# Kernel tuning notes

Hardware: AMD Instinct MI355X
Metric: run time of the kernel (lower is better)

The kernel has to match this reference:

```python
import jax, jax.numpy as jnp
import numpy as np

N = 50000   # nodes
E = 600000  # edges
D = 128     # hidden dim (all layers)
LN_EPS = 1e-5


def setup_inputs() -> dict:
    key = jax.random.key(0)
    ks = jax.random.split(key, 12)
    s = 1.0 / np.sqrt(D)
    inp = {
        "x": jax.random.normal(ks[0], (N, D), jnp.float32),
        "edge_index": jax.random.randint(ks[1], (2, E), 0, N, dtype=jnp.int64),
    }
    # per-layer params: SAGEConv lin_l (W+b, applied to aggregated neighbors),
    # lin_r (W only, applied to root/self), LayerNorm gamma/beta
    for i in range(2):
        inp[f"W_l{i}"] = jax.random.normal(ks[2 + 5 * i], (D, D), jnp.float32) * s
        inp[f"b_l{i}"] = jnp.zeros((D,), jnp.float32)
        inp[f"W_r{i}"] = jax.random.normal(ks[3 + 5 * i], (D, D), jnp.float32) * s
        inp[f"gamma{i}"] = jnp.ones((D,), jnp.float32)
        inp[f"beta{i}"] = jnp.zeros((D,), jnp.float32)
    return inp


def _sage_layer(x, src, dst, W_l, b_l, W_r, gamma, beta):
    n = x.shape[0]
    # mean-aggregate source features at destination nodes (PyG SAGEConv 'mean')
    msg = x[src]                                                # [E, D] gather
    summed = jax.ops.segment_sum(msg, dst, num_segments=n)      # [N, D] scatter-add
    cnt = jax.ops.segment_sum(jnp.ones_like(dst, dtype=x.dtype), dst, num_segments=n)
    agg = summed / jnp.maximum(cnt, 1.0)[:, None]               # zero for isolated nodes
    out = agg @ W_l.T + b_l + x @ W_r.T                         # lin_l(agg) + lin_r(x)
    # LayerNorm + ReLU (dropout=None, negative_slope=None -> ReLU)
    mu = jnp.mean(out, axis=-1, keepdims=True)
    var = jnp.var(out, axis=-1, keepdims=True)
    out = (out - mu) * jax.lax.rsqrt(var + LN_EPS) * gamma + beta
    return jax.nn.relu(out)


def reference(x, edge_index, W_l0, b_l0, W_r0, gamma0, beta0,
              W_l1, b_l1, W_r1, gamma1, beta1):
    src, dst = edge_index[0], edge_index[1]
    x = _sage_layer(x, src, dst, W_l0, b_l0, W_r0, gamma0, beta0)
    x = _sage_layer(x, src, dst, W_l1, b_l1, W_r1, gamma1, beta1)
    return x
```

## Files before the change

### kernel.cpp

```cpp
#include <hip/hip_runtime.h>

#define D 128
#define BR 128

typedef _Float16 f16;
typedef f16 f16x8 __attribute__((ext_vector_type(8)));
typedef float f32x4 __attribute__((ext_vector_type(4)));

__global__ void zero_kernel(int4* __restrict__ p, int count4) {
    const int i = blockIdx.x * 256 + threadIdx.x;
    if (i < count4) p[i] = make_int4(0, 0, 0, 0);
}

__global__ void convert_kernel(const float* __restrict__ src, f16* __restrict__ dst,
                               int count8) {
    const int i = blockIdx.x * 256 + threadIdx.x;
    if (i >= count8) return;
    const float4 v0 = *(const float4*)(src + (size_t)i * 8);
    const float4 v1 = *(const float4*)(src + (size_t)i * 8 + 4);
    f16x8 h;
    h[0] = (f16)v0.x; h[1] = (f16)v0.y; h[2] = (f16)v0.z; h[3] = (f16)v0.w;
    h[4] = (f16)v1.x; h[5] = (f16)v1.y; h[6] = (f16)v1.z; h[7] = (f16)v1.w;
    *(f16x8*)(dst + (size_t)i * 8) = h;
}

__global__ void count_kernel(const int* __restrict__ dst, int* __restrict__ cnt, int E) {
    int e = blockIdx.x * 256 + threadIdx.x;
    if (e < E) atomicAdd(&cnt[dst[e]], 1);
}

__global__ __launch_bounds__(256)
void scan1_kernel(const int* __restrict__ cnt, int* __restrict__ part, int n) {
    const int t = threadIdx.x;
    const int i0 = blockIdx.x * 1024 + t * 4;
    int s = 0;
#pragma unroll
    for (int j = 0; j < 4; ++j) { int i = i0 + j; if (i < n) s += cnt[i]; }
#pragma unroll
    for (int m = 1; m < 64; m <<= 1) s += __shfl_xor(s, m, 64);
    __shared__ int ws[4];
    if ((t & 63) == 0) ws[t >> 6] = s;
    __syncthreads();
    if (t == 0) part[blockIdx.x] = ws[0] + ws[1] + ws[2] + ws[3];
}

__global__ __launch_bounds__(256)
void scan3_kernel(const int* __restrict__ cnt, const int* __restrict__ part,
                  int* __restrict__ off, int* __restrict__ cursor, int n, int nb) {
    const int t = threadIdx.x;
    const int lane = t & 63, wid = t >> 6;
    __shared__ int s_base;
    if (t < 64) {
        int s = 0;
        for (int base = 0; base < nb; base += 64) {
            const int idx = base + lane;
            if (idx < nb && idx < (int)blockIdx.x) s += part[idx];
        }
#pragma unroll
        for (int m = 1; m < 64; m <<= 1) s += __shfl_xor(s, m, 64);
        if (lane == 0) s_base = s;
    }
    const int i0 = blockIdx.x * 1024 + t * 4;
    int v[4]; int s = 0;
#pragma unroll
    for (int j = 0; j < 4; ++j) { v[j] = (i0 + j < n) ? cnt[i0 + j] : 0; s += v[j]; }
    int incl = s;
#pragma unroll
    for (int m = 1; m < 64; m <<= 1) {
        int u = __shfl_up(incl, m, 64);
        if (lane >= m) incl += u;
    }
    __shared__ int ws[4];
    if (lane == 63) ws[wid] = incl;
    __syncthreads();
    int woff = 0;
#pragma unroll
    for (int k = 0; k < 4; ++k) woff += (k < wid) ? ws[k] : 0;
    int run = s_base + woff + incl - s;
#pragma unroll
    for (int j = 0; j < 4; ++j) {
        if (i0 + j < n) { off[i0 + j] = run; cursor[i0 + j] = run; run += v[j]; }
    }
}

__global__ void fill_kernel(const int* __restrict__ src, const int* __restrict__ dst,
                            int* cursor, int* __restrict__ adj, int E) {
    int e = blockIdx.x * 256 + threadIdx.x;
    if (e < E) {
        int pos = atomicAdd(&cursor[dst[e]], 1);
        adj[pos] = src[e];
    }
}

__global__ __launch_bounds__(256, 8)
void aggregate_kernel(const f16* xin, const int* __restrict__ adj,
                      const int* __restrict__ off, const int* __restrict__ cnt,
                      f16* __restrict__ agg, int n) {
    const int node = blockIdx.x * 16 + (threadIdx.x >> 4);
    if (node >= n) return;
    const int lane = threadIdx.x & 15;
    const int deg = cnt[node];
    const int o = off[node];
    const f16* xp = xin + (lane << 3);
    float a0 = 0.f, a1 = 0.f, a2 = 0.f, a3 = 0.f;
    float a4 = 0.f, a5 = 0.f, a6 = 0.f, a7 = 0.f;
    int k = 0;
    for (; k + 8 <= deg; k += 8) {
        int sidx[8];
#pragma unroll
        for (int j = 0; j < 8; ++j) sidx[j] = adj[o + k + j];
#pragma unroll
        for (int j = 0; j < 8; ++j) {
            const f16x8 v = *(const f16x8*)(xp + (size_t)sidx[j] * D);
            a0 += (float)v[0]; a1 += (float)v[1]; a2 += (float)v[2]; a3 += (float)v[3];
            a4 += (float)v[4]; a5 += (float)v[5]; a6 += (float)v[6]; a7 += (float)v[7];
        }
    }
    for (; k + 4 <= deg; k += 4) {
        int sidx[4];
#pragma unroll
        for (int j = 0; j < 4; ++j) sidx[j] = adj[o + k + j];
#pragma unroll
        for (int j = 0; j < 4; ++j) {
            const f16x8 v = *(const f16x8*)(xp + (size_t)sidx[j] * D);
            a0 += (float)v[0]; a1 += (float)v[1]; a2 += (float)v[2]; a3 += (float)v[3];
            a4 += (float)v[4]; a5 += (float)v[5]; a6 += (float)v[6]; a7 += (float)v[7];
        }
    }
    for (; k < deg; ++k) {
        const f16x8 v = *(const f16x8*)(xp + (size_t)adj[o + k] * D);
        a0 += (float)v[0]; a1 += (float)v[1]; a2 += (float)v[2]; a3 += (float)v[3];
        a4 += (float)v[4]; a5 += (float)v[5]; a6 += (float)v[6]; a7 += (float)v[7];
    }
    const float s = 1.0f / (float)max(deg, 1);
    f16x8 r;
    r[0] = (f16)(a0 * s); r[1] = (f16)(a1 * s);
    r[2] = (f16)(a2 * s); r[3] = (f16)(a3 * s);
    r[4] = (f16)(a4 * s); r[5] = (f16)(a5 * s);
    r[6] = (f16)(a6 * s); r[7] = (f16)(a7 * s);
    *(f16x8*)(agg + (size_t)node * D + (lane << 3)) = r;
}

__device__ __forceinline__ void stage_tile_h(const f16* src, f16* dst,
                                             int row0, int n, int tid) {
#pragma unroll
    for (int i = 0; i < 4; ++i) {
        const int flat = i * 4096 + tid * 8;
        const int row = flat >> 7;
        const int k = flat & 127;
        f16x8 h = {};
        if (row0 + row < n) h = *(const f16x8*)(src + (size_t)(row0 + row) * D + k);
        *(f16x8*)(dst + row * D + (k ^ ((row & 7) * 8))) = h;
    }
}

__device__ __forceinline__ void stage_w(const float* __restrict__ src, f16* dst, int tid) {
#pragma unroll
    for (int i = 0; i < 4; ++i) {
        const int flat = i * 4096 + tid * 8;
        const int row = flat >> 7;
        const int k = flat & 127;
        const float4 v0 = *(const float4*)(src + flat);
        const float4 v1 = *(const float4*)(src + flat + 4);
        f16x8 h;
        h[0] = (f16)v0.x; h[1] = (f16)v0.y; h[2] = (f16)v0.z; h[3] = (f16)v0.w;
        h[4] = (f16)v1.x; h[5] = (f16)v1.y; h[6] = (f16)v1.z; h[7] = (f16)v1.w;
        *(f16x8*)(dst + row * D + (k ^ ((row & 7) * 8))) = h;
    }
}

template <bool LAST>
__global__ __launch_bounds__(512, 2)
void fused_kernel(const f16* __restrict__ aggh, const f16* xinh,
                  const float* __restrict__ Wl, const float* __restrict__ bl,
                  const float* __restrict__ Wr,
                  const float* __restrict__ gamma, const float* __restrict__ beta,
                  f16* yh, float* __restrict__ yf, int n) {
    extern __shared__ char lds_raw[];
    f16* As = (f16*)lds_raw;
    f16* Ws = (f16*)(lds_raw + 32768);
    const int tid = threadIdx.x;
    const int w = tid >> 6, l = tid & 63;
    const int c = l & 15, g = l >> 4;
    const int row0 = blockIdx.x * BR;

    f32x4 acc[8];
#pragma unroll
    for (int jt = 0; jt < 8; ++jt) acc[jt] = (f32x4){0.f, 0.f, 0.f, 0.f};

    for (int pass = 0; pass < 2; ++pass) {
        if (pass) __syncthreads();
        stage_tile_h(pass ? xinh : aggh, As, row0, n, tid);
        stage_w(pass ? Wr : Wl, Ws, tid);
        __syncthreads();
#pragma unroll
        for (int ks = 0; ks < 4; ++ks) {
            const int ke = ks * 32 + g * 8;
            const int ar = w * 16 + c;
            const f16x8 av = *(const f16x8*)(As + ar * D + (ke ^ ((ar & 7) * 8)));
            f16x8 bv[8];
#pragma unroll
            for (int jt = 0; jt < 8; ++jt) {
                const int br = jt * 16 + c;
                bv[jt] = *(const f16x8*)(Ws + br * D + (ke ^ ((br & 7) * 8)));
            }
#pragma unroll
            for (int jt = 0; jt < 8; ++jt)
                acc[jt] = __builtin_amdgcn_mfma_f32_16x16x32_f16(
                    av, bv[jt], acc[jt], 0, 0, 0);
        }
    }

    float bj[8], gj[8], btj[8];
#pragma unroll
    for (int jt = 0; jt < 8; ++jt) {
        const int j = jt * 16 + c;
        bj[jt] = bl[j]; gj[jt] = gamma[j]; btj[jt] = beta[j];
    }
#pragma unroll
    for (int reg = 0; reg < 4; ++reg) {
        float v[8]; float s1 = 0.f, s2 = 0.f;
#pragma unroll
        for (int jt = 0; jt < 8; ++jt) {
            v[jt] = acc[jt][reg] + bj[jt];
            s1 += v[jt];
            s2 = fmaf(v[jt], v[jt], s2);
        }
#pragma unroll
        for (int m = 1; m < 16; m <<= 1) {
            s1 += __shfl_xor(s1, m, 64);
            s2 += __shfl_xor(s2, m, 64);
        }
        const float mu = s1 * (1.f / 128.f);
        const float var = s2 * (1.f / 128.f) - mu * mu;
        const float rstd = rsqrtf(var + 1e-5f);
        const int row = row0 + w * 16 + g * 4 + reg;
        if (row < n) {
#pragma unroll
            for (int jt = 0; jt < 8; ++jt) {
                const float o = fmaxf((v[jt] - mu) * rstd * gj[jt] + btj[jt], 0.f);
                if (LAST) yf[(size_t)row * D + jt * 16 + c] = o;
                else      yh[(size_t)row * D + jt * 16 + c] = (f16)o;
            }
        }
    }
}

extern "C" void kernel_launch(void* const* d_in, const int* in_sizes, int n_in,
                              void* d_out, int out_size, void* d_ws, size_t ws_size,
                              hipStream_t stream) {
    const float* x   = (const float*)d_in[0];
    const int*   ei  = (const int*)d_in[1];
    const int E = in_sizes[1] / 2;
    const int n = in_sizes[0] / D;
    const int* srcp = ei;
    const int* dstp = ei + E;
    const float* Wl0 = (const float*)d_in[2];
    const float* bl0 = (const float*)d_in[3];
    const float* Wr0 = (const float*)d_in[4];
    const float* g0  = (const float*)d_in[5];
    const float* be0 = (const float*)d_in[6];
    const float* Wl1 = (const float*)d_in[7];
    const float* bl1 = (const float*)d_in[8];
    const float* Wr1 = (const float*)d_in[9];
    const float* g1  = (const float*)d_in[10];
    const float* be1 = (const float*)d_in[11];
    float* y = (float*)d_out;

    char* ws = (char*)d_ws;
    const size_t aN = ((size_t)n * 4 + 255) & ~(size_t)255;
    const size_t aE = ((size_t)E * 4 + 255) & ~(size_t)255;
    const size_t aP = 4096;
    const size_t aH = ((size_t)n * D * 2 + 255) & ~(size_t)255;
    int* cnt    = (int*)ws;
    int* off    = (int*)(ws + aN);
    int* cursor = (int*)(ws + 2 * aN);
    int* part   = (int*)(ws + 3 * aN);
    int* adj    = (int*)(ws + 3 * aN + aP);
    f16* aggh   = (f16*)(ws + 3 * aN + aP + aE);
    f16* xh     = (f16*)(ws + 3 * aN + aP + aE + aH);
    const size_t need = 3 * aN + aP + aE + 2 * aH;
    if (ws_size < need) return;

    const int LDS_BYTES = 65536;
    hipFuncSetAttribute((const void*)fused_kernel<false>,
                        hipFuncAttributeMaxDynamicSharedMemorySize, LDS_BYTES);
    hipFuncSetAttribute((const void*)fused_kernel<true>,
                        hipFuncAttributeMaxDynamicSharedMemorySize, LDS_BYTES);

    const int gE = (E + 255) / 256;
    const int gA = (n + 15) / 16;
    const int gF = (n + BR - 1) / BR;
    const int nb = (n + 1023) / 1024;
    const int gC = ((n * D / 8) + 255) / 256;
    const int gZ = ((n + 3) / 4 + 255) / 256;

    zero_kernel<<<gZ, 256, 0, stream>>>((int4*)cnt, (n + 3) / 4);
    convert_kernel<<<gC, 256, 0, stream>>>(x, xh, n * D / 8);
    count_kernel<<<gE, 256, 0, stream>>>(dstp, cnt, E);
    scan1_kernel<<<nb, 256, 0, stream>>>(cnt, part, n);
    scan3_kernel<<<nb, 256, 0, stream>>>(cnt, part, off, cursor, n, nb);
    fill_kernel<<<gE, 256, 0, stream>>>(srcp, dstp, cursor, adj, E);

    aggregate_kernel<<<gA, 256, 0, stream>>>(xh, adj, off, cnt, aggh, n);
    fused_kernel<false><<<gF, 512, LDS_BYTES, stream>>>(aggh, xh, Wl0, bl0, Wr0,
                                                        g0, be0, xh, nullptr, n);
    aggregate_kernel<<<gA, 256, 0, stream>>>(xh, adj, off, cnt, aggh, n);
    fused_kernel<true><<<gF, 512, LDS_BYTES, stream>>>(aggh, xh, Wl1, bl1, Wr1,
                                                       g1, be1, nullptr, y, n);
}
```

Baseline: 154.9 us.

## Merge prep kernels, pre-convert weights to fp16, stage tiles via global_load_lds

Folds the count zeroing, the x conversion and a new conversion of all four weight matrices to fp16 into a single grid-stride prep kernel, which removes one launch. The fused GEMM kernel now loads fp16 weights and activation tiles straight into LDS with global_load_lds 16-byte DMA, using an XOR swizzle on the source column. This drops the per-block fp32 weight conversion and the register round trip during staging. The trade-off is an extra workspace buffer and reliance on the LDS layout that the direct load produces per wave. Rows past the end are clamped to n-1 rather than zero-filled.

New measurement: 145.6 us. 1.06x faster.

```diff
diff --git a/kernel.cpp b/kernel.cpp
--- a/kernel.cpp
+++ b/kernel.cpp
@@ -7,21 +7,43 @@
 typedef f16 f16x8 __attribute__((ext_vector_type(8)));
 typedef float f32x4 __attribute__((ext_vector_type(4)));
 
-__global__ void zero_kernel(int4* __restrict__ p, int count4) {
-    const int i = blockIdx.x * 256 + threadIdx.x;
-    if (i < count4) p[i] = make_int4(0, 0, 0, 0);
-}
-
-__global__ void convert_kernel(const float* __restrict__ src, f16* __restrict__ dst,
-                               int count8) {
-    const int i = blockIdx.x * 256 + threadIdx.x;
-    if (i >= count8) return;
-    const float4 v0 = *(const float4*)(src + (size_t)i * 8);
-    const float4 v1 = *(const float4*)(src + (size_t)i * 8 + 4);
-    f16x8 h;
-    h[0] = (f16)v0.x; h[1] = (f16)v0.y; h[2] = (f16)v0.z; h[3] = (f16)v0.w;
-    h[4] = (f16)v1.x; h[5] = (f16)v1.y; h[6] = (f16)v1.z; h[7] = (f16)v1.w;
-    *(f16x8*)(dst + (size_t)i * 8) = h;
+__device__ __forceinline__ void gl_lds16(const f16* g, f16* l) {
+    __builtin_amdgcn_global_load_lds(
+        (const __attribute__((address_space(1))) void*)g,
+        (__attribute__((address_space(3))) void*)l, 16, 0, 0);
+}
+
+__global__ __launch_bounds__(256)
+void prep_kernel(const float* __restrict__ x,
+                 const float* __restrict__ Wl0, const float* __restrict__ Wr0,
+                 const float* __restrict__ Wl1, const float* __restrict__ Wr1,
+                 f16* __restrict__ xh, f16* __restrict__ wh,
+                 int4* __restrict__ cnt4, int nc4, int nx8) {
+    const int nw8 = 2048;
+    const int total = nc4 + nx8 + 4 * nw8;
+    for (int i = blockIdx.x * 256 + threadIdx.x; i < total; i += gridDim.x * 256) {
+        if (i < nc4) {
+            cnt4[i] = make_int4(0, 0, 0, 0);
+        } else if (i < nc4 + nx8) {
+            const int j = i - nc4;
+            const float4 v0 = *(const float4*)(x + (size_t)j * 8);
+            const float4 v1 = *(const float4*)(x + (size_t)j * 8 + 4);
+            f16x8 h;
+            h[0] = (f16)v0.x; h[1] = (f16)v0.y; h[2] = (f16)v0.z; h[3] = (f16)v0.w;
+            h[4] = (f16)v1.x; h[5] = (f16)v1.y; h[6] = (f16)v1.z; h[7] = (f16)v1.w;
+            *(f16x8*)(xh + (size_t)j * 8) = h;
+        } else {
+            const int j = i - nc4 - nx8;
+            const int m = j >> 11, o = j & 2047;
+            const float* Wsrc = (m == 0) ? Wl0 : (m == 1) ? Wr0 : (m == 2) ? Wl1 : Wr1;
+            const float4 v0 = *(const float4*)(Wsrc + o * 8);
+            const float4 v1 = *(const float4*)(Wsrc + o * 8 + 4);
+            f16x8 h;
+            h[0] = (f16)v0.x; h[1] = (f16)v0.y; h[2] = (f16)v0.z; h[3] = (f16)v0.w;
+            h[4] = (f16)v1.x; h[5] = (f16)v1.y; h[6] = (f16)v1.z; h[7] = (f16)v1.w;
+            *(f16x8*)(wh + m * 16384 + o * 8) = h;
+        }
+    }
 }
 
 __global__ void count_kernel(const int* __restrict__ dst, int* __restrict__ cnt, int E) {
@@ -141,39 +163,11 @@
     *(f16x8*)(agg + (size_t)node * D + (lane << 3)) = r;
 }
 
-__device__ __forceinline__ void stage_tile_h(const f16* src, f16* dst,
-                                             int row0, int n, int tid) {
-#pragma unroll
-    for (int i = 0; i < 4; ++i) {
-        const int flat = i * 4096 + tid * 8;
-        const int row = flat >> 7;
-        const int k = flat & 127;
-        f16x8 h = {};
-        if (row0 + row < n) h = *(const f16x8*)(src + (size_t)(row0 + row) * D + k);
-        *(f16x8*)(dst + row * D + (k ^ ((row & 7) * 8))) = h;
-    }
-}
-
-__device__ __forceinline__ void stage_w(const float* __restrict__ src, f16* dst, int tid) {
-#pragma unroll
-    for (int i = 0; i < 4; ++i) {
-        const int flat = i * 4096 + tid * 8;
-        const int row = flat >> 7;
-        const int k = flat & 127;
-        const float4 v0 = *(const float4*)(src + flat);
-        const float4 v1 = *(const float4*)(src + flat + 4);
-        f16x8 h;
-        h[0] = (f16)v0.x; h[1] = (f16)v0.y; h[2] = (f16)v0.z; h[3] = (f16)v0.w;
-        h[4] = (f16)v1.x; h[5] = (f16)v1.y; h[6] = (f16)v1.z; h[7] = (f16)v1.w;
-        *(f16x8*)(dst + row * D + (k ^ ((row & 7) * 8))) = h;
-    }
-}
-
 template <bool LAST>
 __global__ __launch_bounds__(512, 2)
 void fused_kernel(const f16* __restrict__ aggh, const f16* xinh,
-                  const float* __restrict__ Wl, const float* __restrict__ bl,
-                  const float* __restrict__ Wr,
+                  const f16* __restrict__ Whl, const float* __restrict__ bl,
+                  const f16* __restrict__ Whr,
                   const float* __restrict__ gamma, const float* __restrict__ beta,
                   f16* yh, float* __restrict__ yf, int n) {
     extern __shared__ char lds_raw[];
@@ -182,6 +176,7 @@
     const int tid = threadIdx.x;
     const int w = tid >> 6, l = tid & 63;
     const int c = l & 15, g = l >> 4;
+    const int lrow = l >> 4, kgs = l & 15;
     const int row0 = blockIdx.x * BR;
 
     f32x4 acc[8];
@@ -190,8 +185,18 @@
 
     for (int pass = 0; pass < 2; ++pass) {
         if (pass) __syncthreads();
-        stage_tile_h(pass ? xinh : aggh, As, row0, n, tid);
-        stage_w(pass ? Wr : Wl, Ws, tid);
+        const f16* Ain = pass ? xinh : aggh;
+        const f16* Win = pass ? Whr : Whl;
+#pragma unroll
+        for (int i = 0; i < 4; ++i) {
+            const int rbase = i * 32 + w * 4;
+            const int row = rbase + lrow;
+            const int kg = kgs ^ (row & 7);
+            int srow = row0 + row;
+            if (srow >= n) srow = n - 1;
+            gl_lds16(Ain + (size_t)srow * D + kg * 8, As + rbase * D);
+            gl_lds16(Win + row * D + kg * 8, Ws + rbase * D);
+        }
         __syncthreads();
 #pragma unroll
         for (int ks = 0; ks < 4; ++ks) {
@@ -271,15 +276,17 @@
     const size_t aN = ((size_t)n * 4 + 255) & ~(size_t)255;
     const size_t aE = ((size_t)E * 4 + 255) & ~(size_t)255;
     const size_t aP = 4096;
+    const size_t aW = 4 * 16384 * 2;
     const size_t aH = ((size_t)n * D * 2 + 255) & ~(size_t)255;
     int* cnt    = (int*)ws;
     int* off    = (int*)(ws + aN);
     int* cursor = (int*)(ws + 2 * aN);
     int* part   = (int*)(ws + 3 * aN);
     int* adj    = (int*)(ws + 3 * aN + aP);
-    f16* aggh   = (f16*)(ws + 3 * aN + aP + aE);
-    f16* xh     = (f16*)(ws + 3 * aN + aP + aE + aH);
-    const size_t need = 3 * aN + aP + aE + 2 * aH;
+    f16* wh     = (f16*)(ws + 3 * aN + aP + aE);
+    f16* aggh   = (f16*)(ws + 3 * aN + aP + aE + aW);
+    f16* xh     = (f16*)(ws + 3 * aN + aP + aE + aW + aH);
+    const size_t need = 3 * aN + aP + aE + aW + 2 * aH;
     if (ws_size < need) return;
 
     const int LDS_BYTES = 65536;
@@ -292,20 +299,22 @@
     const int gA = (n + 15) / 16;
     const int gF = (n + BR - 1) / BR;
     const int nb = (n + 1023) / 1024;
-    const int gC = ((n * D / 8) + 255) / 256;
-    const int gZ = ((n + 3) / 4 + 255) / 256;
-
-    zero_kernel<<<gZ, 256, 0, stream>>>((int4*)cnt, (n + 3) / 4);
-    convert_kernel<<<gC, 256, 0, stream>>>(x, xh, n * D / 8);
+    const int nc4 = (n + 3) / 4;
+    const int nx8 = n * D / 8;
+
+    prep_kernel<<<1024, 256, 0, stream>>>(x, Wl0, Wr0, Wl1, Wr1, xh, wh,
+                                          (int4*)cnt, nc4, nx8);
     count_kernel<<<gE, 256, 0, stream>>>(dstp, cnt, E);
     scan1_kernel<<<nb, 256, 0, stream>>>(cnt, part, n);
     scan3_kernel<<<nb, 256, 0, stream>>>(cnt, part, off, cursor, n, nb);
     fill_kernel<<<gE, 256, 0, stream>>>(srcp, dstp, cursor, adj, E);
 
     aggregate_kernel<<<gA, 256, 0, stream>>>(xh, adj, off, cnt, aggh, n);
-    fused_kernel<false><<<gF, 512, LDS_BYTES, stream>>>(aggh, xh, Wl0, bl0, Wr0,
-                                                        g0, be0, xh, nullptr, n);
+    fused_kernel<false><<<gF, 512, LDS_BYTES, stream>>>(aggh, xh, wh, bl0,
+                                                        wh + 16384, g0, be0,
+                                                        xh, nullptr, n);
     aggregate_kernel<<<gA, 256, 0, stream>>>(xh, adj, off, cnt, aggh, n);
-    fused_kernel<true><<<gF, 512, LDS_BYTES, stream>>>(aggh, xh, Wl1, bl1, Wr1,
-                                                       g1, be1, nullptr, y, n);
-}
+    fused_kernel<true><<<gF, 512, LDS_BYTES, stream>>>(aggh, xh, wh + 32768, bl1,
+                                                       wh + 49152, g1, be1,
+                                                       nullptr, y, n);
+}
```
